# Kernel optimization log

Measured on AMD Instinct MI355X. Metric: run time of the kernel, lower is better.

Reference implementation:

```python
import jax, jax.numpy as jnp
import numpy as np

NUM_HEADS = 4   # num_heads init kwarg
KERNEL = 7      # kernel_size init kwarg
EPS = 1e-5      # nn.LayerNorm default eps


def setup_inputs() -> dict:
    key = jax.random.key(0)
    ks = jax.random.split(key, 6)
    C, depth = 128, 2
    x = jax.random.normal(ks[0], (2, C, 64, 64), jnp.float32)
    qkv_w = jax.random.normal(ks[1], (depth, 3 * C, C), jnp.float32) * 0.05
    qkv_b = jnp.zeros((depth, 3 * C), jnp.float32)
    rpb = jax.random.normal(ks[2], (depth, NUM_HEADS, 2 * KERNEL - 1, 2 * KERNEL - 1), jnp.float32) * 0.02
    proj_w = jax.random.normal(ks[3], (depth, C, C), jnp.float32) * 0.05
    proj_b = jnp.zeros((depth, C), jnp.float32)
    ln_g = jnp.ones((C,), jnp.float32)
    ln_b = jnp.zeros((C,), jnp.float32)
    return dict(x=x, qkv_w=qkv_w, qkv_b=qkv_b, rpb=rpb,
                proj_w=proj_w, proj_b=proj_b, ln_g=ln_g, ln_b=ln_b)


def _na2d(x, w_qkv, b_qkv, rpb, w_p, b_p):
    """NATTEN-style 2D neighborhood attention. x: (B,H,W,C)."""
    B, H, W, C = x.shape
    h, k = NUM_HEADS, KERNEL
    d = C // h
    qkv = (x @ w_qkv.T + b_qkv).reshape(B, H, W, 3, h, d)
    q = qkv[..., 0, :, :] * (d ** -0.5)   # (B,H,W,h,d)
    kk = qkv[..., 1, :, :]
    v = qkv[..., 2, :, :]
    # edge-clamped window starts: each query sees exactly k x k neighbors
    si = jnp.clip(jnp.arange(H) - k // 2, 0, H - k)
    sj = jnp.clip(jnp.arange(W) - k // 2, 0, W - k)
    idx_i = si[:, None] + jnp.arange(k)   # (H,k) absolute row indices
    idx_j = sj[:, None] + jnp.arange(k)   # (W,k) absolute col indices

    def win(t):  # (B,H,W,h,d) -> (B,H,W,k,k,h,d)
        t = t[:, idx_i]          # (B,H,k,W,h,d)
        t = t[:, :, :, idx_j]    # (B,H,k,W,k,h,d)
        return jnp.transpose(t, (0, 1, 3, 2, 4, 5, 6))

    kw = win(kk)
    vw = win(v)
    attn = jnp.einsum('bijhd,bijpqhd->bijhpq', q, kw)  # (B,H,W,h,k,k)
    # relative position bias: index = (neighbor_abs - query) + (k-1)
    bi = jnp.arange(k)[None, :] + (k - 1) - (jnp.arange(H) - si)[:, None]  # (H,k)
    bj = jnp.arange(k)[None, :] + (k - 1) - (jnp.arange(W) - sj)[:, None]  # (W,k)
    bias = rpb[:, bi[:, None, :, None], bj[None, :, None, :]]  # (h,H,W,k,k)
    attn = attn + jnp.transpose(bias, (1, 2, 0, 3, 4))[None]
    attn = jax.nn.softmax(attn.reshape(B, H, W, h, k * k), axis=-1).reshape(B, H, W, h, k, k)
    out = jnp.einsum('bijhpq,bijpqhd->bijhd', attn, vw).reshape(B, H, W, C)
    return out @ w_p.T + b_p


def reference(x, qkv_w, qkv_b, rpb, proj_w, proj_b, ln_g, ln_b):
    y = jnp.transpose(x, (0, 2, 3, 1))  # NCHW -> NHWC
    for l in range(qkv_w.shape[0]):     # depth=2 stacked NA layers
        y = _na2d(y, qkv_w[l], qkv_b[l], rpb[l], proj_w[l], proj_b[l])
    mu = y.mean(-1, keepdims=True)
    var = y.var(-1, keepdims=True)
    y = (y - mu) / jnp.sqrt(var + EPS) * ln_g + ln_b
    return jnp.transpose(y, (0, 3, 1, 2))  # NHWC -> NCHW
```

## Files before the change

### kernel.cpp

```cpp
#include <hip/hip_runtime.h>
#include <hip/hip_bf16.h>
#include <math.h>

#define PIX 8192
typedef __hip_bfloat16 bf16;
typedef __attribute__((ext_vector_type(8))) short short8;
typedef __attribute__((ext_vector_type(4))) float f32x4;

__device__ inline float bflo(unsigned u) { return __uint_as_float(u << 16); }
__device__ inline float bfhi(unsigned u) { return __uint_as_float(u & 0xffff0000u); }
__device__ inline unsigned short f2b(float f) {
  __hip_bfloat16 h = __float2bfloat16(f);
  return *reinterpret_cast<unsigned short*>(&h);
}
__device__ inline unsigned pack2(float a, float b) {
  return (unsigned)f2b(a) | ((unsigned)f2b(b) << 16);
}
__device__ inline short8 ldw8(const float* __restrict__ p) {
  f32x4 lo = *(const f32x4*)p;
  f32x4 hi = *(const f32x4*)(p + 4);
  short8 r;
  r[0] = (short)f2b(lo[0]); r[1] = (short)f2b(lo[1]);
  r[2] = (short)f2b(lo[2]); r[3] = (short)f2b(lo[3]);
  r[4] = (short)f2b(hi[0]); r[5] = (short)f2b(hi[1]);
  r[6] = (short)f2b(hi[2]); r[7] = (short)f2b(hi[3]);
  return r;
}

__global__ __launch_bounds__(256) void xqkv_cvt(const float* __restrict__ x,
                                                const float* __restrict__ qw,
                                                const float* __restrict__ qb,
                                                unsigned short* __restrict__ qkv,
                                                const float* __restrict__ pw,
                                                unsigned short* __restrict__ wq1,
                                                unsigned short* __restrict__ wp) {
  if (blockIdx.x >= 512) {
    int idx = (blockIdx.x - 512) * 256 + threadIdx.x;
    wq1[idx] = f2b(qw[49152 + idx]);
    wq1[idx + 16384] = f2b(qw[49152 + idx + 16384]);
    if (idx < 16384) wq1[idx + 32768] = f2b(qw[49152 + idx + 32768]);
    wp[idx] = f2b(pw[idx]);
    return;
  }

  __shared__ __align__(16) unsigned short As[16 * 136];
  int m0 = blockIdx.x * 16;
  int tid = threadIdx.x;
  int b = m0 >> 12, i = (m0 >> 6) & 63, j0 = m0 & 63;

  for (int idx = tid; idx < 2048; idx += 256) {
    int c = idx >> 4, jl = idx & 15;
    As[jl * 136 + c] =
        f2b(x[(size_t)b * 524288 + (size_t)c * 4096 + i * 64 + j0 + jl]);
  }
  __syncthreads();

  int w = tid >> 6, lane = tid & 63;
  int quad = lane >> 4, l16 = lane & 15;
  short8 a[4];
#pragma unroll
  for (int kc = 0; kc < 4; ++kc)
    a[kc] = *(const short8*)(As + l16 * 136 + kc * 32 + quad * 8);
#pragma unroll
  for (int nt = 0; nt < 6; ++nt) {
    int col = w * 96 + nt * 16 + l16;
    const float* wrow = qw + (size_t)col * 128 + quad * 8;
    f32x4 c = {0.f, 0.f, 0.f, 0.f};
#pragma unroll
    for (int kc = 0; kc < 4; ++kc)
      c = __builtin_amdgcn_mfma_f32_16x16x32_bf16(a[kc], ldw8(wrow + kc * 32), c, 0, 0, 0);
    float bv = qb[col];
#pragma unroll
    for (int r2 = 0; r2 < 4; ++r2)
      qkv[(size_t)(m0 + quad * 4 + r2) * 384 + col] = f2b(c[r2] + bv);
  }
}

#define RSTRIDE 136
template <int MODE>
__global__ __launch_bounds__(512, 2) void attnproj(const unsigned short* __restrict__ qkvp,
                                                   const float* __restrict__ rpb,
                                                   const unsigned short* __restrict__ wp,
                                                   const float* __restrict__ pbias,
                                                   const unsigned short* __restrict__ wq1,
                                                   const float* __restrict__ qb1,
                                                   unsigned short* __restrict__ qkvo,
                                                   const float* __restrict__ g,
                                                   const float* __restrict__ bta,
                                                   float* __restrict__ out) {
  __shared__ __align__(16) unsigned short kbuf[140 * RSTRIDE];
  __shared__ __align__(16) unsigned short vbuf[140 * RSTRIDE];
  __shared__ float rb[676];

  int ti = blockIdx.x >> 4, tj = blockIdx.x & 15;
  int bz = blockIdx.y;
  int tid = threadIdx.x;
  int bi0 = ti * 8 - 3, bj0 = tj * 4 - 3;

  int r = tid & 3;
  int hh = (tid >> 2) & 3;
  int px = tid >> 4;
  int pi = px >> 2, pj = px & 3;
  int i = ti * 8 + pi, j = tj * 4 + pj;
  int pix = (bz * 64 + i) * 64 + j;
  uint4 qt = *(const uint4*)(qkvp + (size_t)pix * 384 + hh * 32 + r * 8);

  for (int t = tid; t < 676; t += 512) rb[t] = rpb[t];

  for (int t = tid; t < 4480; t += 512) {
    int row = t >> 5;
    int sub = t & 31;
    int isv = sub >> 4;
    int c = sub & 15;
    int ri = row / 10, rj = row - ri * 10;
    int gi = bi0 + ri, gj = bj0 + rj;
    uint4 val = make_uint4(0, 0, 0, 0);
    if ((unsigned)gi < 64u && (unsigned)gj < 64u) {
      int pixn = (bz * 64 + gi) * 64 + gj;
      val = *(const uint4*)(qkvp + (size_t)pixn * 384 + 128 + isv * 128 + c * 8);
    }
    *(uint4*)((isv ? vbuf : kbuf) + row * RSTRIDE + c * 8) = val;
  }
  __syncthreads();

  int si = min(max(i - 3, 0), 57), sj = min(max(j - 3, 0), 57);
  int li = si - bi0, lj = sj - bj0;
  int oi = i - si, oj = j - sj;

  const float scale = 0.17677669529663687f;
  float q[8];
  q[0] = bflo(qt.x) * scale;  q[1] = bfhi(qt.x) * scale;
  q[2] = bflo(qt.y) * scale;  q[3] = bfhi(qt.y) * scale;
  q[4] = bflo(qt.z) * scale;  q[5] = bfhi(qt.z) * scale;
  q[6] = bflo(qt.w) * scale;  q[7] = bfhi(qt.w) * scale;

  const unsigned short* kh = kbuf + hh * 32 + r * 8;
  const unsigned short* vh = vbuf + hh * 32 + r * 8;
  const float* rbh = rb + hh * 169;

  int lane = tid & 63;
  float pl[13];
  pl[12] = -INFINITY;
#pragma unroll
  for (int pp = 0; pp < 7; ++pp) {
#pragma unroll
    for (int qq = 0; qq < 7; ++qq) {
      int n = pp * 7 + qq;
      int nn = (li + pp) * 10 + (lj + qq);
      uint4 t = *(const uint4*)(kh + nn * RSTRIDE);
      float dot = q[0] * bflo(t.x) + q[1] * bfhi(t.x)
                + q[2] * bflo(t.y) + q[3] * bfhi(t.y)
                + q[4] * bflo(t.z) + q[5] * bfhi(t.z)
                + q[6] * bflo(t.w) + q[7] * bfhi(t.w);
      dot += __shfl_xor(dot, 1);
      dot += __shfl_xor(dot, 2);
      float val = dot + rbh[(pp + 6 - oi) * 13 + (qq + 6 - oj)];
      if ((n & 3) == r) pl[n >> 2] = val;
    }
  }

  float m = -INFINITY;
#pragma unroll
  for (int idx = 0; idx < 13; ++idx) m = fmaxf(m, pl[idx]);
  m = fmaxf(m, __shfl_xor(m, 1));
  m = fmaxf(m, __shfl_xor(m, 2));

  float sum = 0.f;
  float acc[8] = {0.f, 0.f, 0.f, 0.f, 0.f, 0.f, 0.f, 0.f};
  int lbase = lane & ~3;
#pragma unroll
  for (int pp = 0; pp < 7; ++pp) {
#pragma unroll
    for (int qq = 0; qq < 7; ++qq) {
      int n = pp * 7 + qq;
      float eo = __expf(pl[n >> 2] - m);
      float e = __shfl(eo, lbase | (n & 3));
      sum += e;
      int nn = (li + pp) * 10 + (lj + qq);
      uint4 t = *(const uint4*)(vh + nn * RSTRIDE);
      acc[0] += e * bflo(t.x);  acc[1] += e * bfhi(t.x);
      acc[2] += e * bflo(t.y);  acc[3] += e * bfhi(t.y);
      acc[4] += e * bflo(t.z);  acc[5] += e * bfhi(t.z);
      acc[6] += e * bflo(t.w);  acc[7] += e * bfhi(t.w);
    }
  }
  float inv = 1.f / sum;
  uint4 t;
  t.x = pack2(acc[0] * inv, acc[1] * inv);
  t.y = pack2(acc[2] * inv, acc[3] * inv);
  t.z = pack2(acc[4] * inv, acc[5] * inv);
  t.w = pack2(acc[6] * inv, acc[7] * inv);
  __syncthreads();
  unsigned short* obuf = kbuf;
  *(uint4*)(obuf + px * RSTRIDE + hh * 32 + r * 8) = t;
  __syncthreads();

  unsigned short* ybuf = vbuf;
  int w = tid >> 6;
  int quad = lane >> 4, l16 = lane & 15;
  int mt = w & 1;
  int ng = w >> 1;
  {
    short8 a[4];
#pragma unroll
    for (int kc = 0; kc < 4; ++kc)
      a[kc] = *(const short8*)(obuf + (mt * 16 + l16) * RSTRIDE + kc * 32 + quad * 8);
#pragma unroll
    for (int s = 0; s < 2; ++s) {
      int col = (ng * 2 + s) * 16 + l16;
      const short8* bp = (const short8*)(wp + (size_t)col * 128 + quad * 8);
      f32x4 c = {0.f, 0.f, 0.f, 0.f};
#pragma unroll
      for (int kc = 0; kc < 4; ++kc)
        c = __builtin_amdgcn_mfma_f32_16x16x32_bf16(a[kc], bp[kc * 4], c, 0, 0, 0);
      float bv = pbias[col];
#pragma unroll
      for (int r2 = 0; r2 < 4; ++r2)
        ybuf[(mt * 16 + quad * 4 + r2) * RSTRIDE + col] = f2b(c[r2] + bv);
    }
  }
  __syncthreads();

  if constexpr (MODE == 0) {
    short8 ay[2][4];
#pragma unroll
    for (int mt2 = 0; mt2 < 2; ++mt2)
#pragma unroll
      for (int kc = 0; kc < 4; ++kc)
        ay[mt2][kc] = *(const short8*)(ybuf + (mt2 * 16 + l16) * RSTRIDE + kc * 32 + quad * 8);
#pragma unroll
    for (int s = 0; s < 3; ++s) {
      int col = (w * 3 + s) * 16 + l16;
      const short8* bp = (const short8*)(wq1 + (size_t)col * 128 + quad * 8);
      float bv = qb1[col];
#pragma unroll
      for (int mt2 = 0; mt2 < 2; ++mt2) {
        f32x4 c = {0.f, 0.f, 0.f, 0.f};
#pragma unroll
        for (int kc = 0; kc < 4; ++kc)
          c = __builtin_amdgcn_mfma_f32_16x16x32_bf16(ay[mt2][kc], bp[kc * 4], c, 0, 0, 0);
#pragma unroll
        for (int r2 = 0; r2 < 4; ++r2) {
          int mloc = mt2 * 16 + quad * 4 + r2;
          int gpix = (bz * 64 + ti * 8 + (mloc >> 2)) * 64 + tj * 4 + (mloc & 3);
          qkvo[(size_t)gpix * 384 + col] = f2b(c[r2] + bv);
        }
      }
    }
  } else {
    int px2 = tid >> 4, sub = tid & 15;
    uint4 tv = *(const uint4*)(ybuf + px2 * RSTRIDE + sub * 8);
    float v[8];
    v[0] = bflo(tv.x); v[1] = bfhi(tv.x); v[2] = bflo(tv.y); v[3] = bfhi(tv.y);
    v[4] = bflo(tv.z); v[5] = bfhi(tv.z); v[6] = bflo(tv.w); v[7] = bfhi(tv.w);
    float sum2 = 0.f, sumsq = 0.f;
#pragma unroll
    for (int k = 0; k < 8; ++k) { sum2 += v[k]; sumsq += v[k] * v[k]; }
    sum2 += __shfl_xor(sum2, 1);  sumsq += __shfl_xor(sumsq, 1);
    sum2 += __shfl_xor(sum2, 2);  sumsq += __shfl_xor(sumsq, 2);
    sum2 += __shfl_xor(sum2, 4);  sumsq += __shfl_xor(sumsq, 4);
    sum2 += __shfl_xor(sum2, 8);  sumsq += __shfl_xor(sumsq, 8);
    float mu = sum2 * (1.f / 128.f);
    float rstd = rsqrtf(sumsq * (1.f / 128.f) - mu * mu + 1e-5f);
    int i2 = ti * 8 + (px2 >> 2), j2 = tj * 4 + (px2 & 3);
    int c0 = sub * 8;
    f32x4 g0 = *(const f32x4*)(g + c0),   g1 = *(const f32x4*)(g + c0 + 4);
    f32x4 b0 = *(const f32x4*)(bta + c0), b1 = *(const f32x4*)(bta + c0 + 4);
#pragma unroll
    for (int k = 0; k < 8; ++k) {
      float gg = (k < 4) ? g0[k] : g1[k - 4];
      float bb = (k < 4) ? b0[k] : b1[k - 4];
      float o = (v[k] - mu) * rstd * gg + bb;
      out[(((size_t)bz * 128 + c0 + k) * 64 + i2) * 64 + j2] = o;
    }
  }
}

extern "C" void kernel_launch(void* const* d_in, const int* in_sizes, int n_in,
                              void* d_out, int out_size, void* d_ws, size_t ws_size,
                              hipStream_t stream) {
  (void)in_sizes; (void)n_in; (void)out_size; (void)ws_size;
  const float* x   = (const float*)d_in[0];
  const float* qw  = (const float*)d_in[1];
  const float* qb  = (const float*)d_in[2];
  const float* rpb = (const float*)d_in[3];
  const float* pw  = (const float*)d_in[4];
  const float* pb  = (const float*)d_in[5];
  const float* lg  = (const float*)d_in[6];
  const float* lb  = (const float*)d_in[7];

  unsigned short* qkvA = (unsigned short*)d_ws;
  unsigned short* qkvB = qkvA + (size_t)PIX * 384;
  unsigned short* wq1  = qkvB + (size_t)PIX * 384;
  unsigned short* wp   = wq1 + 49152;
  float* out = (float*)d_out;

  xqkv_cvt<<<640, 256, 0, stream>>>(x, qw, qb, qkvA, pw, wq1, wp);
  attnproj<0><<<dim3(128, 2), 512, 0, stream>>>(qkvA, rpb, wp, pb, wq1,
                                                qb + 384, qkvB, nullptr,
                                                nullptr, nullptr);
  attnproj<1><<<dim3(128, 2), 512, 0, stream>>>(qkvB, rpb + 676, wp + 16384,
                                                pb + 128, nullptr, nullptr,
                                                nullptr, lg, lb, out);
}
```

Before: 126.6 us.

## Double threads per attention block, splitting head dim across 8 lanes

Doubles the attention/projection block from 512 to 1024 threads. Each thread now handles 4 head channels instead of 8, with 8 lanes per head and an extra shuffle level. The projection and next-layer QKV MFMA work is redistributed so each of the 16 waves does one tile per output group, and LayerNorm runs on half the threads. The goal is more latency hiding within each block on a grid of only 256 blocks. The cost is more shuffles and per-element overhead, plus tighter register limits from the launch bounds.

```diff
diff --git a/kernel.cpp b/kernel.cpp
--- a/kernel.cpp
+++ b/kernel.cpp
@@ -78,16 +78,16 @@
 
 #define RSTRIDE 136
 template <int MODE>
-__global__ __launch_bounds__(512, 2) void attnproj(const unsigned short* __restrict__ qkvp,
-                                                   const float* __restrict__ rpb,
-                                                   const unsigned short* __restrict__ wp,
-                                                   const float* __restrict__ pbias,
-                                                   const unsigned short* __restrict__ wq1,
-                                                   const float* __restrict__ qb1,
-                                                   unsigned short* __restrict__ qkvo,
-                                                   const float* __restrict__ g,
-                                                   const float* __restrict__ bta,
-                                                   float* __restrict__ out) {
+__global__ __launch_bounds__(1024, 4) void attnproj(const unsigned short* __restrict__ qkvp,
+                                                    const float* __restrict__ rpb,
+                                                    const unsigned short* __restrict__ wp,
+                                                    const float* __restrict__ pbias,
+                                                    const unsigned short* __restrict__ wq1,
+                                                    const float* __restrict__ qb1,
+                                                    unsigned short* __restrict__ qkvo,
+                                                    const float* __restrict__ g,
+                                                    const float* __restrict__ bta,
+                                                    float* __restrict__ out) {
   __shared__ __align__(16) unsigned short kbuf[140 * RSTRIDE];
   __shared__ __align__(16) unsigned short vbuf[140 * RSTRIDE];
   __shared__ float rb[676];
@@ -97,17 +97,17 @@
   int tid = threadIdx.x;
   int bi0 = ti * 8 - 3, bj0 = tj * 4 - 3;
 
-  int r = tid & 3;
-  int hh = (tid >> 2) & 3;
-  int px = tid >> 4;
+  int r = tid & 7;
+  int hh = (tid >> 3) & 3;
+  int px = tid >> 5;
   int pi = px >> 2, pj = px & 3;
   int i = ti * 8 + pi, j = tj * 4 + pj;
   int pix = (bz * 64 + i) * 64 + j;
-  uint4 qt = *(const uint4*)(qkvp + (size_t)pix * 384 + hh * 32 + r * 8);
-
-  for (int t = tid; t < 676; t += 512) rb[t] = rpb[t];
-
-  for (int t = tid; t < 4480; t += 512) {
+  uint2 qt = *(const uint2*)(qkvp + (size_t)pix * 384 + hh * 32 + r * 4);
+
+  if (tid < 676) rb[tid] = rpb[tid];
+
+  for (int t = tid; t < 4480; t += 1024) {
     int row = t >> 5;
     int sub = t & 31;
     int isv = sub >> 4;
@@ -128,150 +128,138 @@
   int oi = i - si, oj = j - sj;
 
   const float scale = 0.17677669529663687f;
-  float q[8];
+  float q[4];
   q[0] = bflo(qt.x) * scale;  q[1] = bfhi(qt.x) * scale;
   q[2] = bflo(qt.y) * scale;  q[3] = bfhi(qt.y) * scale;
-  q[4] = bflo(qt.z) * scale;  q[5] = bfhi(qt.z) * scale;
-  q[6] = bflo(qt.w) * scale;  q[7] = bfhi(qt.w) * scale;
-
-  const unsigned short* kh = kbuf + hh * 32 + r * 8;
-  const unsigned short* vh = vbuf + hh * 32 + r * 8;
+
+  const unsigned short* kh = kbuf + hh * 32 + r * 4;
+  const unsigned short* vh = vbuf + hh * 32 + r * 4;
   const float* rbh = rb + hh * 169;
 
   int lane = tid & 63;
-  float pl[13];
-  pl[12] = -INFINITY;
+  float pl[7];
+  pl[6] = -INFINITY;
 #pragma unroll
   for (int pp = 0; pp < 7; ++pp) {
 #pragma unroll
     for (int qq = 0; qq < 7; ++qq) {
       int n = pp * 7 + qq;
       int nn = (li + pp) * 10 + (lj + qq);
-      uint4 t = *(const uint4*)(kh + nn * RSTRIDE);
+      uint2 t = *(const uint2*)(kh + nn * RSTRIDE);
       float dot = q[0] * bflo(t.x) + q[1] * bfhi(t.x)
-                + q[2] * bflo(t.y) + q[3] * bfhi(t.y)
-                + q[4] * bflo(t.z) + q[5] * bfhi(t.z)
-                + q[6] * bflo(t.w) + q[7] * bfhi(t.w);
+                + q[2] * bflo(t.y) + q[3] * bfhi(t.y);
       dot += __shfl_xor(dot, 1);
       dot += __shfl_xor(dot, 2);
+      dot += __shfl_xor(dot, 4);
       float val = dot + rbh[(pp + 6 - oi) * 13 + (qq + 6 - oj)];
-      if ((n & 3) == r) pl[n >> 2] = val;
+      if ((n & 7) == r) pl[n >> 3] = val;
     }
   }
 
   float m = -INFINITY;
 #pragma unroll
-  for (int idx = 0; idx < 13; ++idx) m = fmaxf(m, pl[idx]);
+  for (int idx = 0; idx < 7; ++idx) m = fmaxf(m, pl[idx]);
   m = fmaxf(m, __shfl_xor(m, 1));
   m = fmaxf(m, __shfl_xor(m, 2));
+  m = fmaxf(m, __shfl_xor(m, 4));
 
   float sum = 0.f;
-  float acc[8] = {0.f, 0.f, 0.f, 0.f, 0.f, 0.f, 0.f, 0.f};
-  int lbase = lane & ~3;
+  float acc[4] = {0.f, 0.f, 0.f, 0.f};
+  int lbase = lane & ~7;
 #pragma unroll
   for (int pp = 0; pp < 7; ++pp) {
 #pragma unroll
     for (int qq = 0; qq < 7; ++qq) {
       int n = pp * 7 + qq;
-      float eo = __expf(pl[n >> 2] - m);
-      float e = __shfl(eo, lbase | (n & 3));
+      float eo = __expf(pl[n >> 3] - m);
+      float e = __shfl(eo, lbase | (n & 7));
       sum += e;
       int nn = (li + pp) * 10 + (lj + qq);
-      uint4 t = *(const uint4*)(vh + nn * RSTRIDE);
+      uint2 t = *(const uint2*)(vh + nn * RSTRIDE);
       acc[0] += e * bflo(t.x);  acc[1] += e * bfhi(t.x);
       acc[2] += e * bflo(t.y);  acc[3] += e * bfhi(t.y);
-      acc[4] += e * bflo(t.z);  acc[5] += e * bfhi(t.z);
-      acc[6] += e * bflo(t.w);  acc[7] += e * bfhi(t.w);
     }
   }
   float inv = 1.f / sum;
-  uint4 t;
-  t.x = pack2(acc[0] * inv, acc[1] * inv);
-  t.y = pack2(acc[2] * inv, acc[3] * inv);
-  t.z = pack2(acc[4] * inv, acc[5] * inv);
-  t.w = pack2(acc[6] * inv, acc[7] * inv);
+  uint2 t2;
+  t2.x = pack2(acc[0] * inv, acc[1] * inv);
+  t2.y = pack2(acc[2] * inv, acc[3] * inv);
   __syncthreads();
   unsigned short* obuf = kbuf;
-  *(uint4*)(obuf + px * RSTRIDE + hh * 32 + r * 8) = t;
+  *(uint2*)(obuf + px * RSTRIDE + hh * 32 + r * 4) = t2;
   __syncthreads();
 
   unsigned short* ybuf = vbuf;
   int w = tid >> 6;
   int quad = lane >> 4, l16 = lane & 15;
   int mt = w & 1;
-  int ng = w >> 1;
+  int nt = w >> 1;
   {
     short8 a[4];
 #pragma unroll
     for (int kc = 0; kc < 4; ++kc)
       a[kc] = *(const short8*)(obuf + (mt * 16 + l16) * RSTRIDE + kc * 32 + quad * 8);
-#pragma unroll
-    for (int s = 0; s < 2; ++s) {
-      int col = (ng * 2 + s) * 16 + l16;
-      const short8* bp = (const short8*)(wp + (size_t)col * 128 + quad * 8);
-      f32x4 c = {0.f, 0.f, 0.f, 0.f};
-#pragma unroll
-      for (int kc = 0; kc < 4; ++kc)
-        c = __builtin_amdgcn_mfma_f32_16x16x32_bf16(a[kc], bp[kc * 4], c, 0, 0, 0);
-      float bv = pbias[col];
-#pragma unroll
-      for (int r2 = 0; r2 < 4; ++r2)
-        ybuf[(mt * 16 + quad * 4 + r2) * RSTRIDE + col] = f2b(c[r2] + bv);
-    }
+    int col = nt * 16 + l16;
+    const short8* bp = (const short8*)(wp + (size_t)col * 128 + quad * 8);
+    f32x4 c = {0.f, 0.f, 0.f, 0.f};
+#pragma unroll
+    for (int kc = 0; kc < 4; ++kc)
+      c = __builtin_amdgcn_mfma_f32_16x16x32_bf16(a[kc], bp[kc * 4], c, 0, 0, 0);
+    float bv = pbias[col];
+#pragma unroll
+    for (int r2 = 0; r2 < 4; ++r2)
+      ybuf[(mt * 16 + quad * 4 + r2) * RSTRIDE + col] = f2b(c[r2] + bv);
   }
   __syncthreads();
 
   if constexpr (MODE == 0) {
-    short8 ay[2][4];
-#pragma unroll
-    for (int mt2 = 0; mt2 < 2; ++mt2)
-#pragma unroll
-      for (int kc = 0; kc < 4; ++kc)
-        ay[mt2][kc] = *(const short8*)(ybuf + (mt2 * 16 + l16) * RSTRIDE + kc * 32 + quad * 8);
+    short8 ay[4];
+#pragma unroll
+    for (int kc = 0; kc < 4; ++kc)
+      ay[kc] = *(const short8*)(ybuf + (mt * 16 + l16) * RSTRIDE + kc * 32 + quad * 8);
 #pragma unroll
     for (int s = 0; s < 3; ++s) {
-      int col = (w * 3 + s) * 16 + l16;
+      int col = (nt + 8 * s) * 16 + l16;
       const short8* bp = (const short8*)(wq1 + (size_t)col * 128 + quad * 8);
       float bv = qb1[col];
-#pragma unroll
-      for (int mt2 = 0; mt2 < 2; ++mt2) {
-        f32x4 c = {0.f, 0.f, 0.f, 0.f};
-#pragma unroll
-        for (int kc = 0; kc < 4; ++kc)
-          c = __builtin_amdgcn_mfma_f32_16x16x32_bf16(ay[mt2][kc], bp[kc * 4], c, 0, 0, 0);
-#pragma unroll
-        for (int r2 = 0; r2 < 4; ++r2) {
-          int mloc = mt2 * 16 + quad * 4 + r2;
-          int gpix = (bz * 64 + ti * 8 + (mloc >> 2)) * 64 + tj * 4 + (mloc & 3);
-          qkvo[(size_t)gpix * 384 + col] = f2b(c[r2] + bv);
-        }
+      f32x4 c = {0.f, 0.f, 0.f, 0.f};
+#pragma unroll
+      for (int kc = 0; kc < 4; ++kc)
+        c = __builtin_amdgcn_mfma_f32_16x16x32_bf16(ay[kc], bp[kc * 4], c, 0, 0, 0);
+#pragma unroll
+      for (int r2 = 0; r2 < 4; ++r2) {
+        int mloc = mt * 16 + quad * 4 + r2;
+        int gpix = (bz * 64 + ti * 8 + (mloc >> 2)) * 64 + tj * 4 + (mloc & 3);
+        qkvo[(size_t)gpix * 384 + col] = f2b(c[r2] + bv);
       }
     }
   } else {
-    int px2 = tid >> 4, sub = tid & 15;
-    uint4 tv = *(const uint4*)(ybuf + px2 * RSTRIDE + sub * 8);
-    float v[8];
-    v[0] = bflo(tv.x); v[1] = bfhi(tv.x); v[2] = bflo(tv.y); v[3] = bfhi(tv.y);
-    v[4] = bflo(tv.z); v[5] = bfhi(tv.z); v[6] = bflo(tv.w); v[7] = bfhi(tv.w);
-    float sum2 = 0.f, sumsq = 0.f;
-#pragma unroll
-    for (int k = 0; k < 8; ++k) { sum2 += v[k]; sumsq += v[k] * v[k]; }
-    sum2 += __shfl_xor(sum2, 1);  sumsq += __shfl_xor(sumsq, 1);
-    sum2 += __shfl_xor(sum2, 2);  sumsq += __shfl_xor(sumsq, 2);
-    sum2 += __shfl_xor(sum2, 4);  sumsq += __shfl_xor(sumsq, 4);
-    sum2 += __shfl_xor(sum2, 8);  sumsq += __shfl_xor(sumsq, 8);
-    float mu = sum2 * (1.f / 128.f);
-    float rstd = rsqrtf(sumsq * (1.f / 128.f) - mu * mu + 1e-5f);
-    int i2 = ti * 8 + (px2 >> 2), j2 = tj * 4 + (px2 & 3);
-    int c0 = sub * 8;
-    f32x4 g0 = *(const f32x4*)(g + c0),   g1 = *(const f32x4*)(g + c0 + 4);
-    f32x4 b0 = *(const f32x4*)(bta + c0), b1 = *(const f32x4*)(bta + c0 + 4);
-#pragma unroll
-    for (int k = 0; k < 8; ++k) {
-      float gg = (k < 4) ? g0[k] : g1[k - 4];
-      float bb = (k < 4) ? b0[k] : b1[k - 4];
-      float o = (v[k] - mu) * rstd * gg + bb;
-      out[(((size_t)bz * 128 + c0 + k) * 64 + i2) * 64 + j2] = o;
+    if (tid < 512) {
+      int px2 = tid >> 4, sub = tid & 15;
+      uint4 tv = *(const uint4*)(ybuf + px2 * RSTRIDE + sub * 8);
+      float v[8];
+      v[0] = bflo(tv.x); v[1] = bfhi(tv.x); v[2] = bflo(tv.y); v[3] = bfhi(tv.y);
+      v[4] = bflo(tv.z); v[5] = bfhi(tv.z); v[6] = bflo(tv.w); v[7] = bfhi(tv.w);
+      float sum2 = 0.f, sumsq = 0.f;
+#pragma unroll
+      for (int k = 0; k < 8; ++k) { sum2 += v[k]; sumsq += v[k] * v[k]; }
+      sum2 += __shfl_xor(sum2, 1);  sumsq += __shfl_xor(sumsq, 1);
+      sum2 += __shfl_xor(sum2, 2);  sumsq += __shfl_xor(sumsq, 2);
+      sum2 += __shfl_xor(sum2, 4);  sumsq += __shfl_xor(sumsq, 4);
+      sum2 += __shfl_xor(sum2, 8);  sumsq += __shfl_xor(sumsq, 8);
+      float mu = sum2 * (1.f / 128.f);
+      float rstd = rsqrtf(sumsq * (1.f / 128.f) - mu * mu + 1e-5f);
+      int i2 = ti * 8 + (px2 >> 2), j2 = tj * 4 + (px2 & 3);
+      int c0 = sub * 8;
+      f32x4 g0 = *(const f32x4*)(g + c0),   g1 = *(const f32x4*)(g + c0 + 4);
+      f32x4 b0 = *(const f32x4*)(bta + c0), b1 = *(const f32x4*)(bta + c0 + 4);
+#pragma unroll
+      for (int k = 0; k < 8; ++k) {
+        float gg = (k < 4) ? g0[k] : g1[k - 4];
+        float bb = (k < 4) ? b0[k] : b1[k - 4];
+        float o = (v[k] - mu) * rstd * gg + bb;
+        out[(((size_t)bz * 128 + c0 + k) * 64 + i2) * 64 + j2] = o;
+      }
     }
   }
 }
@@ -296,10 +284,10 @@
   float* out = (float*)d_out;
 
   xqkv_cvt<<<640, 256, 0, stream>>>(x, qw, qb, qkvA, pw, wq1, wp);
-  attnproj<0><<<dim3(128, 2), 512, 0, stream>>>(qkvA, rpb, wp, pb, wq1,
-                                                qb + 384, qkvB, nullptr,
-                                                nullptr, nullptr);
-  attnproj<1><<<dim3(128, 2), 512, 0, stream>>>(qkvB, rpb + 676, wp + 16384,
-                                                pb + 128, nullptr, nullptr,
-                                                nullptr, lg, lb, out);
-}
+  attnproj<0><<<dim3(128, 2), 1024, 0, stream>>>(qkvA, rpb, wp, pb, wq1,
+                                                 qb + 384, qkvB, nullptr,
+                                                 nullptr, nullptr);
+  attnproj<1><<<dim3(128, 2), 1024, 0, stream>>>(qkvB, rpb + 676, wp + 16384,
+                                                 pb + 128, nullptr, nullptr,
+                                                 nullptr, lg, lb, out);
+}
```

After: 132.5 us. 4.7% more time.
